# Optimization experiments

Measured on AMD Instinct MI355X. Metric: run time of the kernel, lower is better.

The kernel has to match this reference:

```python
import jax, jax.numpy as jnp
import numpy as np

N_NODES = 50000
N_EDGES = 800000
IN_F = 128
HID = 128
OUT = 2


def setup_inputs() -> dict:
    key = jax.random.key(0)
    ks = jax.random.split(key, 10)
    x = jax.random.normal(ks[0], (N_NODES, IN_F), dtype=jnp.float32)
    edge_index = jax.random.randint(ks[1], (2, N_EDGES), 0, N_NODES, dtype=jnp.int64)

    def lin(k, fan_in, fan_out):
        s = 1.0 / np.sqrt(fan_in)
        return jax.random.uniform(k, (fan_in, fan_out), jnp.float32, -s, s)

    return {
        "x": x,
        "edge_index": edge_index,
        # SAGEConv1: lin_l applied to mean-aggregated neighbors (with bias),
        # lin_r applied to root features (no bias), PyG convention.
        "W1_l": lin(ks[2], IN_F, HID),
        "W1_r": lin(ks[3], IN_F, HID),
        "b1": jnp.zeros((HID,), jnp.float32),
        "W2_l": lin(ks[4], HID, HID),
        "W2_r": lin(ks[5], HID, HID),
        "b2": jnp.zeros((HID,), jnp.float32),
        "Wfc": lin(ks[6], HID, OUT),
        "bfc": jnp.zeros((OUT,), jnp.float32),
    }


def reference(x, edge_index, W1_l, W1_r, b1, W2_l, W2_r, b2, Wfc, bfc):
    n = x.shape[0]
    src = edge_index[0]  # message source j
    dst = edge_index[1]  # aggregation target i
    # in-degree for mean aggregation (clamp to avoid div-by-zero for isolated nodes)
    deg = jax.ops.segment_sum(jnp.ones_like(dst, dtype=x.dtype), dst, num_segments=n)
    inv_deg = 1.0 / jnp.maximum(deg, 1.0)  # [n]

    def sage_conv(h, Wl, Wr, b):
        # mean over incoming neighbor features, then two linear maps
        agg = jax.ops.segment_sum(h[src], dst, num_segments=n) * inv_deg[:, None]
        return agg @ Wl + h @ Wr + b

    # dropout is identity at inference (training=False)
    h = jax.nn.relu(sage_conv(x, W1_l, W1_r, b1))
    h = jax.nn.relu(sage_conv(h, W2_l, W2_r, b2))
    return h @ Wfc + bfc  # [n, out] logits
```

## Files before the change

### kernel.cpp

```cpp
#include <hip/hip_runtime.h>

#define NN 50000
#define NE 800000
#define DEGCAP 64

#define NXCD 8
#define NPS ((NN + NXCD - 1) / NXCD)
#define SEPB 4096
#define NCHUNK ((NE + SEPB - 1) / SEPB)
#define SCAT_GRID (NCHUNK * NXCD)

#define CVT_BLKS 6250
#define PREP_BLKS 32
#define ZERO_BLKS 50
#define SETUP_GRID (CVT_BLKS + PREP_BLKS + ZERO_BLKS)

typedef short short8 __attribute__((ext_vector_type(8)));
typedef short short4v __attribute__((ext_vector_type(4)));
typedef float f32x4 __attribute__((ext_vector_type(4)));
typedef _Float16 half8v __attribute__((ext_vector_type(8)));

__device__ inline unsigned short f16_bits(float f) {
    _Float16 h = (_Float16)f;
    return __builtin_bit_cast(unsigned short, h);
}

__global__ __launch_bounds__(256) void setup_kernel(const float* __restrict__ x,
                                                    unsigned short* __restrict__ xb,
                                                    const float* __restrict__ W0,
                                                    const float* __restrict__ W1,
                                                    const float* __restrict__ W2,
                                                    const float* __restrict__ W3,
                                                    short* __restrict__ wf,
                                                    int* __restrict__ deg,
                                                    unsigned short* __restrict__ h1b) {
    int b = blockIdx.x;
    if (b < CVT_BLKS) {
        int i = b * 256 + threadIdx.x;
        float4 v = ((const float4*)x)[i];
        short4v r;
        r[0] = (short)f16_bits(v.x);
        r[1] = (short)f16_bits(v.y);
        r[2] = (short)f16_bits(v.z);
        r[3] = (short)f16_bits(v.w);
        ((short4v*)xb)[i] = r;
    } else if (b < CVT_BLKS + PREP_BLKS) {
        int t = (b - CVT_BLKS) * 256 + threadIdx.x;
        int mat = t >> 11;
        const float* W = (mat == 0) ? W0 : (mat == 1) ? W1 : (mat == 2) ? W2 : W3;
        short* out = wf + (size_t)mat * 16384;
        int r = t & 2047;
        int nt = r >> 8;
        int kc = (r >> 6) & 3;
        int lane = r & 63;
        int n = nt * 16 + (lane & 15);
        int kbase = kc * 32 + ((lane >> 4) << 3);
        short8 vh;
#pragma unroll
        for (int j = 0; j < 8; ++j) {
            float w = W[(size_t)(kbase + j) * 128 + n];
            vh[j] = (short)f16_bits(w);
        }
        size_t o = ((size_t)((nt * 4 + kc) * 64 + lane)) * 8;
        *(short8*)(out + o) = vh;
    } else {
        int bl = b - CVT_BLKS - PREP_BLKS;
        int idx = bl * 256 + threadIdx.x;
        if (idx < (NN / 4)) ((int4*)deg)[idx] = make_int4(0, 0, 0, 0);
        if (bl == ZERO_BLKS - 1) {
            int t = threadIdx.x;
            short8 z = {0, 0, 0, 0, 0, 0, 0, 0};
            if (t < 16) *(short8*)(xb + ((size_t)NN << 7) + (t << 3)) = z;
            else if (t < 32) *(short8*)(h1b + ((size_t)NN << 7) + ((t - 16) << 3)) = z;
        }
    }
}

__global__ __launch_bounds__(256) void scatter_kernel(const int* __restrict__ src,
                                                      const int* __restrict__ dst,
                                                      int* __restrict__ deg,
                                                      unsigned short* __restrict__ col, int ne) {
    int slot8 = blockIdx.x & 7;
    int chunk = blockIdx.x >> 3;
    int lo = slot8 * NPS, hi = lo + NPS;
    int base = chunk * SEPB;
    int end = base + SEPB;
    if (end > ne) end = ne;
    for (int i = base + threadIdx.x; i < end; i += 256) {
        int d = dst[i];
        if (d >= lo && d < hi) {
            int s = src[i];
            int sl = atomicAdd(&deg[d], 1);
            col[((size_t)d << 6) + sl] = (unsigned short)s;
        }
    }
}

__global__ __launch_bounds__(256) void agg_kernel(const unsigned short* __restrict__ hb,
                                                  const unsigned short* __restrict__ col,
                                                  const int* __restrict__ deg,
                                                  unsigned short* __restrict__ outb, int n) {
    int node = blockIdx.x * 4 + (threadIdx.x >> 6);
    if (node >= n) return;
    int lane = threadIdx.x & 63;
    int slot = lane >> 4, sub = lane & 15;
    int dg = deg[node];
    const unsigned short* base = hb + (sub << 3);
    const unsigned short* cp = col + ((size_t)node << 6);
    float acc[8];
#pragma unroll
    for (int j = 0; j < 8; ++j) acc[j] = 0.f;

    for (int e0 = slot; e0 < dg; e0 += 16) {
        int c[4];
#pragma unroll
        for (int j = 0; j < 4; ++j) {
            int e = e0 + 4 * j;
            int cc = cp[e < DEGCAP ? e : 0];
            c[j] = (e < dg) ? cc : NN;
        }
        half8v v[4];
#pragma unroll
        for (int j = 0; j < 4; ++j) v[j] = *(const half8v*)(base + ((size_t)c[j] << 7));
        half8v s = (v[0] + v[1]) + (v[2] + v[3]);
#pragma unroll
        for (int q = 0; q < 8; ++q) acc[q] += (float)s[q];
    }
#pragma unroll
    for (int j = 0; j < 8; ++j) {
        acc[j] += __shfl_xor(acc[j], 16, 64);
        acc[j] += __shfl_xor(acc[j], 32, 64);
    }
    if (slot == 0) {
        float s = 1.0f / (float)(dg > 0 ? dg : 1);
        short8 o;
#pragma unroll
        for (int j = 0; j < 8; ++j) o[j] = (short)f16_bits(acc[j] * s);
        *(short8*)(outb + ((size_t)node << 7) + (sub << 3)) = o;
    }
}

__global__ __launch_bounds__(256) void gemm_mfma(const unsigned short* __restrict__ A0b,
                                                 const unsigned short* __restrict__ A1b,
                                                 const short* __restrict__ Wf0,
                                                 const short* __restrict__ Wf1,
                                                 const float* __restrict__ bias,
                                                 unsigned short* __restrict__ outb,
                                                 const float* __restrict__ Wfc,
                                                 const float* __restrict__ bfc,
                                                 float* __restrict__ fcout,
                                                 int n, int relu) {
    int lane = threadIdx.x & 63;
    int wave = threadIdx.x >> 6;
    int quad = lane >> 4, m16 = lane & 15;
    int row_base = blockIdx.x * 64 + wave * 16;
    int arow = row_base + m16;
    if (arow > n - 1) arow = n - 1;

    const unsigned short* ap0 = A0b + ((size_t)arow << 7) + (quad << 3);
    const unsigned short* ap1 = A1b + ((size_t)arow << 7) + (quad << 3);
    half8v a0[4], a1[4];
#pragma unroll
    for (int kc = 0; kc < 4; ++kc) {
        a0[kc] = *(const half8v*)(ap0 + kc * 32);
        a1[kc] = *(const half8v*)(ap1 + kc * 32);
    }

    f32x4 acc[8];
#pragma unroll
    for (int nt = 0; nt < 8; ++nt) acc[nt] = (f32x4){0.f, 0.f, 0.f, 0.f};

#pragma unroll
    for (int kc = 0; kc < 4; ++kc) {
        const short* wp0 = Wf0 + ((size_t)kc * 64 + lane) * 8;
        const short* wp1 = Wf1 + ((size_t)kc * 64 + lane) * 8;
#pragma unroll
        for (int nt = 0; nt < 8; ++nt) {
            half8v b0 = *(const half8v*)(wp0 + (size_t)nt * 2048);
            half8v b1 = *(const half8v*)(wp1 + (size_t)nt * 2048);
            acc[nt] = __builtin_amdgcn_mfma_f32_16x16x32_f16(a0[kc], b0, acc[nt], 0, 0, 0);
            acc[nt] = __builtin_amdgcn_mfma_f32_16x16x32_f16(a1[kc], b1, acc[nt], 0, 0, 0);
        }
    }

    float bcol[8];
#pragma unroll
    for (int nt = 0; nt < 8; ++nt) bcol[nt] = bias[nt * 16 + m16];

    if (Wfc) {
        float w0[8], w1[8];
#pragma unroll
        for (int nt = 0; nt < 8; ++nt) {
            float2 wv = *(const float2*)(Wfc + 2 * (nt * 16 + m16));
            w0[nt] = wv.x;
            w1[nt] = wv.y;
        }
        float b0 = bfc[0], b1 = bfc[1];
#pragma unroll
        for (int r = 0; r < 4; ++r) {
            float p0 = 0.f, p1 = 0.f;
#pragma unroll
            for (int nt = 0; nt < 8; ++nt) {
                float v = fmaxf(acc[nt][r] + bcol[nt], 0.f);
                p0 += v * w0[nt];
                p1 += v * w1[nt];
            }
#pragma unroll
            for (int off = 1; off < 16; off <<= 1) {
                p0 += __shfl_xor(p0, off, 64);
                p1 += __shfl_xor(p1, off, 64);
            }
            int row = row_base + quad * 4 + r;
            if (m16 == 0 && row < n) {
                float2 o;
                o.x = p0 + b0;
                o.y = p1 + b1;
                *(float2*)(fcout + 2 * (size_t)row) = o;
            }
        }
    } else {
#pragma unroll
        for (int r = 0; r < 4; ++r) {
            int row = row_base + quad * 4 + r;
            if (row >= n) continue;
            unsigned short* opb = outb + ((size_t)row << 7) + m16;
#pragma unroll
            for (int nt = 0; nt < 8; ++nt) {
                float v = acc[nt][r] + bcol[nt];
                if (relu) v = fmaxf(v, 0.f);
                opb[nt * 16] = f16_bits(v);
            }
        }
    }
}

extern "C" void kernel_launch(void* const* d_in, const int* in_sizes, int n_in,
                              void* d_out, int out_size, void* d_ws, size_t ws_size,
                              hipStream_t stream) {
    const float* x   = (const float*)d_in[0];
    const int* edge  = (const int*)d_in[1];
    const float* W1l = (const float*)d_in[2];
    const float* W1r = (const float*)d_in[3];
    const float* b1  = (const float*)d_in[4];
    const float* W2l = (const float*)d_in[5];
    const float* W2r = (const float*)d_in[6];
    const float* b2  = (const float*)d_in[7];
    const float* Wfc = (const float*)d_in[8];
    const float* bfc = (const float*)d_in[9];
    float* out = (float*)d_out;

    const int n = NN, ne = NE;
    const int* src = edge;
    const int* dst = edge + ne;

    char* ws = (char*)d_ws;
    size_t off = 0;
    auto alloc = [&](size_t bytes) -> char* {
        char* p = ws + off;
        off = (off + bytes + 511) & ~(size_t)511;
        return p;
    };
    int* deg              = (int*)alloc((size_t)NN * 4);
    short* wf             = (short*)alloc((size_t)4 * 16384 * 2);
    unsigned short* col   = (unsigned short*)alloc((size_t)NN * DEGCAP * 2);
    unsigned short* xb    = (unsigned short*)alloc((size_t)(n + 1) * 128 * 2);
    unsigned short* aggb  = (unsigned short*)alloc((size_t)n * 128 * 2);
    unsigned short* h1b   = (unsigned short*)alloc((size_t)(n + 1) * 128 * 2);
    (void)ws_size; (void)in_sizes; (void)n_in; (void)out_size;

    setup_kernel<<<SETUP_GRID, 256, 0, stream>>>(x, xb, W1l, W1r, W2l, W2r, wf, deg, h1b);
    scatter_kernel<<<SCAT_GRID, 256, 0, stream>>>(src, dst, deg, col, ne);

    agg_kernel<<<(n + 3) / 4, 256, 0, stream>>>(xb, col, deg, aggb, n);
    gemm_mfma<<<(n + 63) / 64, 256, 0, stream>>>(aggb, xb, wf, wf + 16384, b1, h1b,
                                                 (const float*)0, (const float*)0, (float*)0, n, 1);
    agg_kernel<<<(n + 3) / 4, 256, 0, stream>>>(h1b, col, deg, aggb, n);
    gemm_mfma<<<(n + 63) / 64, 256, 0, stream>>>(aggb, h1b, wf + 2 * 16384, wf + 3 * 16384, b2,
                                                 (unsigned short*)0, Wfc, bfc, out, n, 1);
}
```

Measured before the change: 212.4 us.

## Fuse neighbor aggregation into MFMA GEMM and merge scatter into setup kernel

Neighbor mean aggregation now runs inside the MFMA GEMM kernel. Each lane gathers its row's neighbors directly into A-fragment registers, so the intermediate aggregated buffer is no longer written and read back. The edge-scatter work is folded into the setup kernel, and degree zeroing moves to a memset, which cuts the launch count. The cost is a much smaller aggregation grid: each lane walks the full degree of its row serially, where before 16 edge slots per node ran in parallel. That means less parallelism and more load imbalance when hiding gather latency.

```diff
diff --git a/kernel.cpp b/kernel.cpp
--- a/kernel.cpp
+++ b/kernel.cpp
@@ -8,12 +8,10 @@
 #define NPS ((NN + NXCD - 1) / NXCD)
 #define SEPB 4096
 #define NCHUNK ((NE + SEPB - 1) / SEPB)
-#define SCAT_GRID (NCHUNK * NXCD)
-
+#define SCAT_BLKS (NCHUNK * NXCD)
 #define CVT_BLKS 6250
 #define PREP_BLKS 32
-#define ZERO_BLKS 50
-#define SETUP_GRID (CVT_BLKS + PREP_BLKS + ZERO_BLKS)
+#define K1_GRID (SCAT_BLKS + CVT_BLKS + PREP_BLKS + 1)
 
 typedef short short8 __attribute__((ext_vector_type(8)));
 typedef short short4v __attribute__((ext_vector_type(4)));
@@ -25,18 +23,36 @@
     return __builtin_bit_cast(unsigned short, h);
 }
 
-__global__ __launch_bounds__(256) void setup_kernel(const float* __restrict__ x,
-                                                    unsigned short* __restrict__ xb,
-                                                    const float* __restrict__ W0,
-                                                    const float* __restrict__ W1,
-                                                    const float* __restrict__ W2,
-                                                    const float* __restrict__ W3,
-                                                    short* __restrict__ wf,
-                                                    int* __restrict__ deg,
-                                                    unsigned short* __restrict__ h1b) {
+__global__ __launch_bounds__(256) void k1_kernel(const float* __restrict__ x,
+                                                 unsigned short* __restrict__ xb,
+                                                 const float* __restrict__ W0,
+                                                 const float* __restrict__ W1,
+                                                 const float* __restrict__ W2,
+                                                 const float* __restrict__ W3,
+                                                 short* __restrict__ wf,
+                                                 int* __restrict__ deg,
+                                                 unsigned short* __restrict__ col,
+                                                 const int* __restrict__ src,
+                                                 const int* __restrict__ dst,
+                                                 unsigned short* __restrict__ h1b) {
     int b = blockIdx.x;
-    if (b < CVT_BLKS) {
-        int i = b * 256 + threadIdx.x;
+    if (b < SCAT_BLKS) {
+        int slot8 = b & 7;
+        int chunk = b >> 3;
+        int lo = slot8 * NPS, hi = lo + NPS;
+        int base = chunk * SEPB;
+        int end = base + SEPB;
+        if (end > NE) end = NE;
+        for (int i = base + (int)threadIdx.x; i < end; i += 256) {
+            int d = dst[i];
+            if (d >= lo && d < hi) {
+                int s = src[i];
+                int sl = atomicAdd(&deg[d], 1);
+                col[((size_t)d << 6) + sl] = (unsigned short)s;
+            }
+        }
+    } else if (b < SCAT_BLKS + CVT_BLKS) {
+        int i = (b - SCAT_BLKS) * 256 + threadIdx.x;
         float4 v = ((const float4*)x)[i];
         short4v r;
         r[0] = (short)f16_bits(v.x);
@@ -44,8 +60,8 @@
         r[2] = (short)f16_bits(v.z);
         r[3] = (short)f16_bits(v.w);
         ((short4v*)xb)[i] = r;
-    } else if (b < CVT_BLKS + PREP_BLKS) {
-        int t = (b - CVT_BLKS) * 256 + threadIdx.x;
+    } else if (b < SCAT_BLKS + CVT_BLKS + PREP_BLKS) {
+        int t = (b - SCAT_BLKS - CVT_BLKS) * 256 + threadIdx.x;
         int mat = t >> 11;
         const float* W = (mat == 0) ? W0 : (mat == 1) ? W1 : (mat == 2) ? W2 : W3;
         short* out = wf + (size_t)mat * 16384;
@@ -64,107 +80,80 @@
         size_t o = ((size_t)((nt * 4 + kc) * 64 + lane)) * 8;
         *(short8*)(out + o) = vh;
     } else {
-        int bl = b - CVT_BLKS - PREP_BLKS;
-        int idx = bl * 256 + threadIdx.x;
-        if (idx < (NN / 4)) ((int4*)deg)[idx] = make_int4(0, 0, 0, 0);
-        if (bl == ZERO_BLKS - 1) {
-            int t = threadIdx.x;
-            short8 z = {0, 0, 0, 0, 0, 0, 0, 0};
-            if (t < 16) *(short8*)(xb + ((size_t)NN << 7) + (t << 3)) = z;
-            else if (t < 32) *(short8*)(h1b + ((size_t)NN << 7) + ((t - 16) << 3)) = z;
-        }
-    }
-}
-
-__global__ __launch_bounds__(256) void scatter_kernel(const int* __restrict__ src,
-                                                      const int* __restrict__ dst,
-                                                      int* __restrict__ deg,
-                                                      unsigned short* __restrict__ col, int ne) {
-    int slot8 = blockIdx.x & 7;
-    int chunk = blockIdx.x >> 3;
-    int lo = slot8 * NPS, hi = lo + NPS;
-    int base = chunk * SEPB;
-    int end = base + SEPB;
-    if (end > ne) end = ne;
-    for (int i = base + threadIdx.x; i < end; i += 256) {
-        int d = dst[i];
-        if (d >= lo && d < hi) {
-            int s = src[i];
-            int sl = atomicAdd(&deg[d], 1);
-            col[((size_t)d << 6) + sl] = (unsigned short)s;
-        }
-    }
-}
-
-__global__ __launch_bounds__(256) void agg_kernel(const unsigned short* __restrict__ hb,
+        int t = threadIdx.x;
+        short8 z = {0, 0, 0, 0, 0, 0, 0, 0};
+        if (t < 16) *(short8*)(xb + ((size_t)NN << 7) + (t << 3)) = z;
+        else if (t < 32) *(short8*)(h1b + ((size_t)NN << 7) + ((t - 16) << 3)) = z;
+    }
+}
+
+__global__ __launch_bounds__(256) void fused_sage(const unsigned short* __restrict__ hb,
                                                   const unsigned short* __restrict__ col,
                                                   const int* __restrict__ deg,
-                                                  unsigned short* __restrict__ outb, int n) {
-    int node = blockIdx.x * 4 + (threadIdx.x >> 6);
-    if (node >= n) return;
-    int lane = threadIdx.x & 63;
-    int slot = lane >> 4, sub = lane & 15;
-    int dg = deg[node];
-    const unsigned short* base = hb + (sub << 3);
-    const unsigned short* cp = col + ((size_t)node << 6);
-    float acc[8];
-#pragma unroll
-    for (int j = 0; j < 8; ++j) acc[j] = 0.f;
-
-    for (int e0 = slot; e0 < dg; e0 += 16) {
-        int c[4];
-#pragma unroll
-        for (int j = 0; j < 4; ++j) {
-            int e = e0 + 4 * j;
-            int cc = cp[e < DEGCAP ? e : 0];
-            c[j] = (e < dg) ? cc : NN;
-        }
-        half8v v[4];
-#pragma unroll
-        for (int j = 0; j < 4; ++j) v[j] = *(const half8v*)(base + ((size_t)c[j] << 7));
-        half8v s = (v[0] + v[1]) + (v[2] + v[3]);
-#pragma unroll
-        for (int q = 0; q < 8; ++q) acc[q] += (float)s[q];
-    }
-#pragma unroll
-    for (int j = 0; j < 8; ++j) {
-        acc[j] += __shfl_xor(acc[j], 16, 64);
-        acc[j] += __shfl_xor(acc[j], 32, 64);
-    }
-    if (slot == 0) {
-        float s = 1.0f / (float)(dg > 0 ? dg : 1);
-        short8 o;
-#pragma unroll
-        for (int j = 0; j < 8; ++j) o[j] = (short)f16_bits(acc[j] * s);
-        *(short8*)(outb + ((size_t)node << 7) + (sub << 3)) = o;
-    }
-}
-
-__global__ __launch_bounds__(256) void gemm_mfma(const unsigned short* __restrict__ A0b,
-                                                 const unsigned short* __restrict__ A1b,
-                                                 const short* __restrict__ Wf0,
-                                                 const short* __restrict__ Wf1,
-                                                 const float* __restrict__ bias,
-                                                 unsigned short* __restrict__ outb,
-                                                 const float* __restrict__ Wfc,
-                                                 const float* __restrict__ bfc,
-                                                 float* __restrict__ fcout,
-                                                 int n, int relu) {
+                                                  const short* __restrict__ Wf0,
+                                                  const short* __restrict__ Wf1,
+                                                  const float* __restrict__ bias,
+                                                  unsigned short* __restrict__ outb,
+                                                  const float* __restrict__ Wfc,
+                                                  const float* __restrict__ bfc,
+                                                  float* __restrict__ fcout,
+                                                  int relu) {
     int lane = threadIdx.x & 63;
     int wave = threadIdx.x >> 6;
     int quad = lane >> 4, m16 = lane & 15;
     int row_base = blockIdx.x * 64 + wave * 16;
     int arow = row_base + m16;
-    if (arow > n - 1) arow = n - 1;
-
-    const unsigned short* ap0 = A0b + ((size_t)arow << 7) + (quad << 3);
-    const unsigned short* ap1 = A1b + ((size_t)arow << 7) + (quad << 3);
-    half8v a0[4], a1[4];
-#pragma unroll
-    for (int kc = 0; kc < 4; ++kc) {
-        a0[kc] = *(const half8v*)(ap0 + kc * 32);
-        a1[kc] = *(const half8v*)(ap1 + kc * 32);
-    }
+    if (arow > NN - 1) arow = NN - 1;
+
+    int dg = deg[arow];
+    const unsigned short* cp = col + ((size_t)arow << 6);
+    const unsigned short* tq = hb + (quad << 3);
+
+    float accg[4][8];
+#pragma unroll
+    for (int kc = 0; kc < 4; ++kc)
+#pragma unroll
+        for (int j = 0; j < 8; ++j) accg[kc][j] = 0.f;
+
+    int e = 0;
+    for (; e + 4 <= dg; e += 4) {
+        int c0 = cp[e], c1 = cp[e + 1], c2 = cp[e + 2], c3 = cp[e + 3];
+        const unsigned short* r0 = tq + ((size_t)c0 << 7);
+        const unsigned short* r1 = tq + ((size_t)c1 << 7);
+        const unsigned short* r2 = tq + ((size_t)c2 << 7);
+        const unsigned short* r3 = tq + ((size_t)c3 << 7);
+#pragma unroll
+        for (int kc = 0; kc < 4; ++kc) {
+            half8v v0 = *(const half8v*)(r0 + kc * 32);
+            half8v v1 = *(const half8v*)(r1 + kc * 32);
+            half8v v2 = *(const half8v*)(r2 + kc * 32);
+            half8v v3 = *(const half8v*)(r3 + kc * 32);
+            half8v s = (v0 + v1) + (v2 + v3);
+#pragma unroll
+            for (int q = 0; q < 8; ++q) accg[kc][q] += (float)s[q];
+        }
+    }
+    for (; e < dg; ++e) {
+        const unsigned short* r0 = tq + ((size_t)cp[e] << 7);
+#pragma unroll
+        for (int kc = 0; kc < 4; ++kc) {
+            half8v v0 = *(const half8v*)(r0 + kc * 32);
+#pragma unroll
+            for (int q = 0; q < 8; ++q) accg[kc][q] += (float)v0[q];
+        }
+    }
+
+    float sdeg = 1.0f / (float)(dg > 0 ? dg : 1);
+    half8v a0[4];
+#pragma unroll
+    for (int kc = 0; kc < 4; ++kc)
+#pragma unroll
+        for (int j = 0; j < 8; ++j) a0[kc][j] = (_Float16)(accg[kc][j] * sdeg);
+
+    half8v a1[4];
+#pragma unroll
+    for (int kc = 0; kc < 4; ++kc)
+        a1[kc] = *(const half8v*)(hb + ((size_t)arow << 7) + kc * 32 + (quad << 3));
 
     f32x4 acc[8];
 #pragma unroll
@@ -211,7 +200,7 @@
                 p1 += __shfl_xor(p1, off, 64);
             }
             int row = row_base + quad * 4 + r;
-            if (m16 == 0 && row < n) {
+            if (m16 == 0 && row < NN) {
                 float2 o;
                 o.x = p0 + b0;
                 o.y = p1 + b1;
@@ -222,7 +211,7 @@
 #pragma unroll
         for (int r = 0; r < 4; ++r) {
             int row = row_base + quad * 4 + r;
-            if (row >= n) continue;
+            if (row >= NN) continue;
             unsigned short* opb = outb + ((size_t)row << 7) + m16;
 #pragma unroll
             for (int nt = 0; nt < 8; ++nt) {
@@ -249,9 +238,8 @@
     const float* bfc = (const float*)d_in[9];
     float* out = (float*)d_out;
 
-    const int n = NN, ne = NE;
     const int* src = edge;
-    const int* dst = edge + ne;
+    const int* dst = edge + NE;
 
     char* ws = (char*)d_ws;
     size_t off = 0;
@@ -263,18 +251,18 @@
     int* deg              = (int*)alloc((size_t)NN * 4);
     short* wf             = (short*)alloc((size_t)4 * 16384 * 2);
     unsigned short* col   = (unsigned short*)alloc((size_t)NN * DEGCAP * 2);
-    unsigned short* xb    = (unsigned short*)alloc((size_t)(n + 1) * 128 * 2);
-    unsigned short* aggb  = (unsigned short*)alloc((size_t)n * 128 * 2);
-    unsigned short* h1b   = (unsigned short*)alloc((size_t)(n + 1) * 128 * 2);
+    unsigned short* xb    = (unsigned short*)alloc((size_t)(NN + 1) * 128 * 2);
+    unsigned short* h1b   = (unsigned short*)alloc((size_t)(NN + 1) * 128 * 2);
     (void)ws_size; (void)in_sizes; (void)n_in; (void)out_size;
 
-    setup_kernel<<<SETUP_GRID, 256, 0, stream>>>(x, xb, W1l, W1r, W2l, W2r, wf, deg, h1b);
-    scatter_kernel<<<SCAT_GRID, 256, 0, stream>>>(src, dst, deg, col, ne);
-
-    agg_kernel<<<(n + 3) / 4, 256, 0, stream>>>(xb, col, deg, aggb, n);
-    gemm_mfma<<<(n + 63) / 64, 256, 0, stream>>>(aggb, xb, wf, wf + 16384, b1, h1b,
-                                                 (const float*)0, (const float*)0, (float*)0, n, 1);
-    agg_kernel<<<(n + 3) / 4, 256, 0, stream>>>(h1b, col, deg, aggb, n);
-    gemm_mfma<<<(n + 63) / 64, 256, 0, stream>>>(aggb, h1b, wf + 2 * 16384, wf + 3 * 16384, b2,
-                                                 (unsigned short*)0, Wfc, bfc, out, n, 1);
-}
+    hipMemsetAsync(deg, 0, (size_t)NN * 4, stream);
+    k1_kernel<<<K1_GRID, 256, 0, stream>>>(x, xb, W1l, W1r, W2l, W2r, wf,
+                                           deg, col, src, dst, h1b);
+    fused_sage<<<(NN + 63) / 64, 256, 0, stream>>>(xb, col, deg,
+                                                   wf, wf + 16384, b1, h1b,
+                                                   (const float*)0, (const float*)0,
+                                                   (float*)0, 1);
+    fused_sage<<<(NN + 63) / 64, 256, 0, stream>>>(h1b, col, deg,
+                                                   wf + 2 * 16384, wf + 3 * 16384, b2,
+                                                   (unsigned short*)0, Wfc, bfc, out, 0);
+}
```

Result: slower. 222.2 us (+4.6%).

## Bucket neighbor lists by source-node range and fuse scatter into setup kernel

Applied to the files above, without the earlier changes.

Neighbor indices for each destination are now split into four buckets by source-node range, each with its own count and a capacity of 24. The aggregation walks the buckets in order, so the feature-row gathers visit source rows in rough address order, which should improve cache locality. The scatter is merged into the conversion/setup kernel, and the degree zeroing moves to a hipMemsetAsync, removing one kernel launch. The per-bucket cap of 24 could overflow on skewed inputs, and the setup work now runs without ordering against the scatter, which adds bucket-loop overhead in aggregation.

```diff
diff --git a/kernel.cpp b/kernel.cpp
--- a/kernel.cpp
+++ b/kernel.cpp
@@ -2,18 +2,19 @@
 
 #define NN 50000
 #define NE 800000
-#define DEGCAP 64
+#define NCHK 4
+#define CROWS 12500
+#define CCAP 24
+#define CSTRIDE (NCHK * CCAP)
 
 #define NXCD 8
 #define NPS ((NN + NXCD - 1) / NXCD)
 #define SEPB 4096
 #define NCHUNK ((NE + SEPB - 1) / SEPB)
-#define SCAT_GRID (NCHUNK * NXCD)
-
+#define SCAT_BLKS (NCHUNK * NXCD)
 #define CVT_BLKS 6250
 #define PREP_BLKS 32
-#define ZERO_BLKS 50
-#define SETUP_GRID (CVT_BLKS + PREP_BLKS + ZERO_BLKS)
+#define K1_GRID (SCAT_BLKS + CVT_BLKS + PREP_BLKS + 1)
 
 typedef short short8 __attribute__((ext_vector_type(8)));
 typedef short short4v __attribute__((ext_vector_type(4)));
@@ -25,18 +26,37 @@
     return __builtin_bit_cast(unsigned short, h);
 }
 
-__global__ __launch_bounds__(256) void setup_kernel(const float* __restrict__ x,
-                                                    unsigned short* __restrict__ xb,
-                                                    const float* __restrict__ W0,
-                                                    const float* __restrict__ W1,
-                                                    const float* __restrict__ W2,
-                                                    const float* __restrict__ W3,
-                                                    short* __restrict__ wf,
-                                                    int* __restrict__ deg,
-                                                    unsigned short* __restrict__ h1b) {
+__global__ __launch_bounds__(256) void k1_kernel(const float* __restrict__ x,
+                                                 unsigned short* __restrict__ xb,
+                                                 const float* __restrict__ W0,
+                                                 const float* __restrict__ W1,
+                                                 const float* __restrict__ W2,
+                                                 const float* __restrict__ W3,
+                                                 short* __restrict__ wf,
+                                                 int* __restrict__ deg4,
+                                                 unsigned short* __restrict__ col,
+                                                 const int* __restrict__ src,
+                                                 const int* __restrict__ dst,
+                                                 unsigned short* __restrict__ h1b) {
     int b = blockIdx.x;
-    if (b < CVT_BLKS) {
-        int i = b * 256 + threadIdx.x;
+    if (b < SCAT_BLKS) {
+        int slot8 = b & 7;
+        int chunk = b >> 3;
+        int lo = slot8 * NPS, hi = lo + NPS;
+        int base = chunk * SEPB;
+        int end = base + SEPB;
+        if (end > NE) end = NE;
+        for (int i = base + (int)threadIdx.x; i < end; i += 256) {
+            int d = dst[i];
+            if (d >= lo && d < hi) {
+                int s = src[i];
+                int c = s / CROWS;
+                int sl = atomicAdd(&deg4[d * NCHK + c], 1);
+                col[(size_t)d * CSTRIDE + c * CCAP + sl] = (unsigned short)s;
+            }
+        }
+    } else if (b < SCAT_BLKS + CVT_BLKS) {
+        int i = (b - SCAT_BLKS) * 256 + threadIdx.x;
         float4 v = ((const float4*)x)[i];
         short4v r;
         r[0] = (short)f16_bits(v.x);
@@ -44,8 +64,8 @@
         r[2] = (short)f16_bits(v.z);
         r[3] = (short)f16_bits(v.w);
         ((short4v*)xb)[i] = r;
-    } else if (b < CVT_BLKS + PREP_BLKS) {
-        int t = (b - CVT_BLKS) * 256 + threadIdx.x;
+    } else if (b < SCAT_BLKS + CVT_BLKS + PREP_BLKS) {
+        int t = (b - SCAT_BLKS - CVT_BLKS) * 256 + threadIdx.x;
         int mat = t >> 11;
         const float* W = (mat == 0) ? W0 : (mat == 1) ? W1 : (mat == 2) ? W2 : W3;
         short* out = wf + (size_t)mat * 16384;
@@ -64,67 +84,47 @@
         size_t o = ((size_t)((nt * 4 + kc) * 64 + lane)) * 8;
         *(short8*)(out + o) = vh;
     } else {
-        int bl = b - CVT_BLKS - PREP_BLKS;
-        int idx = bl * 256 + threadIdx.x;
-        if (idx < (NN / 4)) ((int4*)deg)[idx] = make_int4(0, 0, 0, 0);
-        if (bl == ZERO_BLKS - 1) {
-            int t = threadIdx.x;
-            short8 z = {0, 0, 0, 0, 0, 0, 0, 0};
-            if (t < 16) *(short8*)(xb + ((size_t)NN << 7) + (t << 3)) = z;
-            else if (t < 32) *(short8*)(h1b + ((size_t)NN << 7) + ((t - 16) << 3)) = z;
-        }
-    }
-}
-
-__global__ __launch_bounds__(256) void scatter_kernel(const int* __restrict__ src,
-                                                      const int* __restrict__ dst,
-                                                      int* __restrict__ deg,
-                                                      unsigned short* __restrict__ col, int ne) {
-    int slot8 = blockIdx.x & 7;
-    int chunk = blockIdx.x >> 3;
-    int lo = slot8 * NPS, hi = lo + NPS;
-    int base = chunk * SEPB;
-    int end = base + SEPB;
-    if (end > ne) end = ne;
-    for (int i = base + threadIdx.x; i < end; i += 256) {
-        int d = dst[i];
-        if (d >= lo && d < hi) {
-            int s = src[i];
-            int sl = atomicAdd(&deg[d], 1);
-            col[((size_t)d << 6) + sl] = (unsigned short)s;
-        }
+        int t = threadIdx.x;
+        short8 z = {0, 0, 0, 0, 0, 0, 0, 0};
+        if (t < 16) *(short8*)(xb + ((size_t)NN << 7) + (t << 3)) = z;
+        else if (t < 32) *(short8*)(h1b + ((size_t)NN << 7) + ((t - 16) << 3)) = z;
     }
 }
 
 __global__ __launch_bounds__(256) void agg_kernel(const unsigned short* __restrict__ hb,
                                                   const unsigned short* __restrict__ col,
-                                                  const int* __restrict__ deg,
+                                                  const int* __restrict__ deg4,
                                                   unsigned short* __restrict__ outb, int n) {
     int node = blockIdx.x * 4 + (threadIdx.x >> 6);
     if (node >= n) return;
     int lane = threadIdx.x & 63;
     int slot = lane >> 4, sub = lane & 15;
-    int dg = deg[node];
     const unsigned short* base = hb + (sub << 3);
-    const unsigned short* cp = col + ((size_t)node << 6);
     float acc[8];
 #pragma unroll
     for (int j = 0; j < 8; ++j) acc[j] = 0.f;
 
-    for (int e0 = slot; e0 < dg; e0 += 16) {
-        int c[4];
-#pragma unroll
-        for (int j = 0; j < 4; ++j) {
-            int e = e0 + 4 * j;
-            int cc = cp[e < DEGCAP ? e : 0];
-            c[j] = (e < dg) ? cc : NN;
-        }
-        half8v v[4];
-#pragma unroll
-        for (int j = 0; j < 4; ++j) v[j] = *(const half8v*)(base + ((size_t)c[j] << 7));
-        half8v s = (v[0] + v[1]) + (v[2] + v[3]);
-#pragma unroll
-        for (int q = 0; q < 8; ++q) acc[q] += (float)s[q];
+    int dtot = 0;
+#pragma unroll
+    for (int c = 0; c < NCHK; ++c) {
+        int dgc = deg4[node * NCHK + c];
+        dtot += dgc;
+        const unsigned short* cp = col + (size_t)node * CSTRIDE + c * CCAP;
+        for (int e0 = slot; e0 < dgc; e0 += 16) {
+            int ci[4];
+#pragma unroll
+            for (int j = 0; j < 4; ++j) {
+                int e = e0 + 4 * j;
+                int cc = cp[e < CCAP ? e : 0];
+                ci[j] = (e < dgc) ? cc : NN;
+            }
+            half8v v[4];
+#pragma unroll
+            for (int j = 0; j < 4; ++j) v[j] = *(const half8v*)(base + ((size_t)ci[j] << 7));
+            half8v s = (v[0] + v[1]) + (v[2] + v[3]);
+#pragma unroll
+            for (int q = 0; q < 8; ++q) acc[q] += (float)s[q];
+        }
     }
 #pragma unroll
     for (int j = 0; j < 8; ++j) {
@@ -132,7 +132,7 @@
         acc[j] += __shfl_xor(acc[j], 32, 64);
     }
     if (slot == 0) {
-        float s = 1.0f / (float)(dg > 0 ? dg : 1);
+        float s = 1.0f / (float)(dtot > 0 ? dtot : 1);
         short8 o;
 #pragma unroll
         for (int j = 0; j < 8; ++j) o[j] = (short)f16_bits(acc[j] * s);
@@ -249,9 +249,9 @@
     const float* bfc = (const float*)d_in[9];
     float* out = (float*)d_out;
 
-    const int n = NN, ne = NE;
+    const int n = NN;
     const int* src = edge;
-    const int* dst = edge + ne;
+    const int* dst = edge + NE;
 
     char* ws = (char*)d_ws;
     size_t off = 0;
@@ -260,21 +260,22 @@
         off = (off + bytes + 511) & ~(size_t)511;
         return p;
     };
-    int* deg              = (int*)alloc((size_t)NN * 4);
+    int* deg4             = (int*)alloc((size_t)NN * NCHK * 4);
     short* wf             = (short*)alloc((size_t)4 * 16384 * 2);
-    unsigned short* col   = (unsigned short*)alloc((size_t)NN * DEGCAP * 2);
-    unsigned short* xb    = (unsigned short*)alloc((size_t)(n + 1) * 128 * 2);
-    unsigned short* aggb  = (unsigned short*)alloc((size_t)n * 128 * 2);
-    unsigned short* h1b   = (unsigned short*)alloc((size_t)(n + 1) * 128 * 2);
+    unsigned short* col   = (unsigned short*)alloc((size_t)NN * CSTRIDE * 2);
+    unsigned short* xb    = (unsigned short*)alloc((size_t)(NN + 1) * 128 * 2);
+    unsigned short* aggb  = (unsigned short*)alloc((size_t)NN * 128 * 2);
+    unsigned short* h1b   = (unsigned short*)alloc((size_t)(NN + 1) * 128 * 2);
     (void)ws_size; (void)in_sizes; (void)n_in; (void)out_size;
 
-    setup_kernel<<<SETUP_GRID, 256, 0, stream>>>(x, xb, W1l, W1r, W2l, W2r, wf, deg, h1b);
-    scatter_kernel<<<SCAT_GRID, 256, 0, stream>>>(src, dst, deg, col, ne);
-
-    agg_kernel<<<(n + 3) / 4, 256, 0, stream>>>(xb, col, deg, aggb, n);
+    hipMemsetAsync(deg4, 0, (size_t)NN * NCHK * 4, stream);
+    k1_kernel<<<K1_GRID, 256, 0, stream>>>(x, xb, W1l, W1r, W2l, W2r, wf,
+                                           deg4, col, src, dst, h1b);
+
+    agg_kernel<<<(n + 3) / 4, 256, 0, stream>>>(xb, col, deg4, aggb, n);
     gemm_mfma<<<(n + 63) / 64, 256, 0, stream>>>(aggb, xb, wf, wf + 16384, b1, h1b,
                                                  (const float*)0, (const float*)0, (float*)0, n, 1);
-    agg_kernel<<<(n + 3) / 4, 256, 0, stream>>>(h1b, col, deg, aggb, n);
+    agg_kernel<<<(n + 3) / 4, 256, 0, stream>>>(h1b, col, deg4, aggb, n);
     gemm_mfma<<<(n + 63) / 64, 256, 0, stream>>>(aggb, h1b, wf + 2 * 16384, wf + 3 * 16384, b2,
                                                  (unsigned short*)0, Wfc, bfc, out, n, 1);
 }
```

After: 240.1 us. 1.13x slower.
